# Performance work log

Hardware: AMD Instinct MI355X
Metric: run time of the kernel (lower is better)

## Reference

```python
import jax, jax.numpy as jnp
import numpy as np

NUM_USERS = 100000
NUM_ITEMS = 50000
EMBED = 64
S_NNZ = NUM_USERS * 32   # avg social degree 32
R_NNZ = NUM_USERS * 50   # avg 50 rated items per user
BATCH = 8192


def setup_inputs() -> dict:
    key = jax.random.key(0)
    ks = jax.random.split(key, 12)
    d = EMBED
    # Embedding tables (xavier-uniform style scale)
    U = jax.random.uniform(ks[0], (NUM_USERS, d), jnp.float32, -1.0, 1.0) * np.sqrt(6.0 / (NUM_USERS + d))
    V = jax.random.uniform(ks[1], (NUM_ITEMS, d), jnp.float32, -1.0, 1.0) * np.sqrt(6.0 / (NUM_ITEMS + d))
    # Diffusion layer weights: Linear(2d -> d). Stored as [2d, d] (x @ W + b).
    lim = np.sqrt(6.0 / (3 * d))
    W0 = jax.random.uniform(ks[2], (2 * d, d), jnp.float32, -lim, lim)
    b0 = jnp.zeros((d,), jnp.float32)
    W1 = jax.random.uniform(ks[3], (2 * d, d), jnp.float32, -lim, lim)
    b1 = jnp.zeros((d,), jnp.float32)
    # Sparse social matrix S [NUM_USERS, NUM_USERS], COO edge lists, row-normalized values.
    S_row = jax.random.randint(ks[4], (S_NNZ,), 0, NUM_USERS, jnp.int32)
    S_col = jax.random.randint(ks[5], (S_NNZ,), 0, NUM_USERS, jnp.int32)
    S_val = jnp.full((S_NNZ,), 1.0 / 32.0, jnp.float32)
    # Sparse rating matrix R [NUM_USERS, NUM_ITEMS]
    R_row = jax.random.randint(ks[6], (R_NNZ,), 0, NUM_USERS, jnp.int32)
    R_col = jax.random.randint(ks[7], (R_NNZ,), 0, NUM_ITEMS, jnp.int32)
    R_val = jnp.full((R_NNZ,), 1.0 / 50.0, jnp.float32)
    batch_user = jax.random.randint(ks[8], (BATCH,), 0, NUM_USERS, jnp.int64 if jax.config.jax_enable_x64 else jnp.int32)
    batch_pos_item = jax.random.randint(ks[9], (BATCH,), 0, NUM_ITEMS, jnp.int32)
    batch_neg_item = jax.random.randint(ks[10], (BATCH,), 0, NUM_ITEMS, jnp.int32)
    return dict(batch_user=batch_user, batch_pos_item=batch_pos_item, batch_neg_item=batch_neg_item,
                U=U, V=V, W0=W0, b0=b0, W1=W1, b1=b1,
                S_row=S_row, S_col=S_col, S_val=S_val,
                R_row=R_row, R_col=R_col, R_val=R_val)


def _spmm(row, col, val, X, n_rows):
    # (sparse [n_rows, n] COO) @ X : gather + scale + segment-sum
    return jax.ops.segment_sum(val[:, None] * X[col], row, num_segments=n_rows)


def reference(batch_user, batch_pos_item, batch_neg_item, U, V, W0, b0, W1, b1,
              S_row, S_col, S_val, R_row, R_col, R_val):
    # Diffusion layers: U <- relu(concat([S @ U, U]) @ W + b)
    for W, b in ((W0, b0), (W1, b1)):
        agg = _spmm(S_row, S_col, S_val, U, NUM_USERS)          # [num_users, d]
        U = jax.nn.relu(jnp.concatenate([agg, U], axis=1) @ W + b)
    user_g = U + _spmm(R_row, R_col, R_val, V, NUM_USERS)        # [num_users, d]
    bu = user_g[batch_user]          # [B, d]
    bp = V[batch_pos_item]           # [B, d]
    bn = V[batch_neg_item]           # [B, d]
    return (bu, bp, bn)
```

## Files before the change

### kernel.cpp

```cpp
#include <hip/hip_runtime.h>
#include <hip/hip_bf16.h>

#define NUM_USERS 100000
#define NUM_ITEMS 50000
#define EMBED     64
#define S_NNZ     (NUM_USERS * 32)
#define R_NNZ     (NUM_USERS * 50)
#define BATCH     8192

#define NB    256
#define NCH   256
#define CHUNK (S_NNZ / NCH)
#define BROWS 391


__global__ __launch_bounds__(256) void k_p1hist(const int* __restrict__ rows, int* __restrict__ cnt_t) {
    __shared__ int h[NB];
    int t = threadIdx.x, b = blockIdx.x;
    h[t] = 0;
    __syncthreads();
    int base = b * CHUNK;
    for (int i = t; i < CHUNK; i += 256) atomicAdd(&h[rows[base + i] / BROWS], 1);
    __syncthreads();
    cnt_t[t * NCH + b] = h[t];
}

__global__ __launch_bounds__(1024) void k_scan1(const int* __restrict__ cnt, int* __restrict__ excl,
                                                int* __restrict__ bsums, int n) {
    __shared__ int buf[1024];
    int t = threadIdx.x;
    int i = blockIdx.x * 1024 + t;
    int x = (i < n) ? cnt[i] : 0;
    buf[t] = x;
    __syncthreads();
    for (int off = 1; off < 1024; off <<= 1) {
        int y = (t >= off) ? buf[t - off] : 0;
        __syncthreads();
        buf[t] += y;
        __syncthreads();
    }
    if (i < n) excl[i] = buf[t] - x;
    if (t == 1023) bsums[blockIdx.x] = buf[1023];
}

__global__ __launch_bounds__(1024) void k_scan2(int* __restrict__ bsums, int nb, int* __restrict__ total_slot) {
    __shared__ int buf[1024];
    int t = threadIdx.x;
    int x = (t < nb) ? bsums[t] : 0;
    buf[t] = x;
    __syncthreads();
    for (int off = 1; off < 1024; off <<= 1) {
        int y = (t >= off) ? buf[t - off] : 0;
        __syncthreads();
        buf[t] += y;
        __syncthreads();
    }
    if (t < nb) bsums[t] = buf[t] - x;
    if (t == 1023) total_slot[0] = buf[1023];
}

__global__ void k_scan3b(int* __restrict__ a, const int* __restrict__ bsums, int n) {
    int i = blockIdx.x * blockDim.x + threadIdx.x;
    if (i < n) a[i] += bsums[i >> 10];
}

__global__ __launch_bounds__(256) void k_p1scatter(const int* __restrict__ rows, const int* __restrict__ cols,
                                                   const float* __restrict__ vals, const int* __restrict__ cnt_t,
                                                   int* __restrict__ tmpRow, int2* __restrict__ tmpCV) {
    __shared__ int cur[NB];
    int t = threadIdx.x, b = blockIdx.x;
    cur[t] = cnt_t[t * NCH + b];
    __syncthreads();
    int base = b * CHUNK;
    for (int i = t; i < CHUNK; i += 256) {
        int e = base + i;
        int r = rows[e];
        int pos = atomicAdd(&cur[r / BROWS], 1);
        tmpRow[pos] = r;
        tmpCV[pos]  = make_int2(cols[e], __float_as_int(vals[e]));
    }
}

__global__ __launch_bounds__(512) void k_p2(const int* __restrict__ tmpRow, const int2* __restrict__ tmpCV,
                                            const int* __restrict__ cnt_t,
                                            int* __restrict__ rowptr, int2* __restrict__ colval) {
    __shared__ int h[512];
    __shared__ int s[512];
    __shared__ int cur[BROWS + 1];
    int t = threadIdx.x, k = blockIdx.x;
    int beg = cnt_t[k * NCH];
    int end = (k < NB - 1) ? cnt_t[(k + 1) * NCH] : S_NNZ;
    h[t] = 0;
    __syncthreads();
    int rbase = k * BROWS;
    for (int j = beg + t; j < end; j += 512) atomicAdd(&h[tmpRow[j] - rbase], 1);
    __syncthreads();
    s[t] = h[t];
    __syncthreads();
    for (int off = 1; off < 512; off <<= 1) {
        int y = (t >= off) ? s[t - off] : 0;
        __syncthreads();
        s[t] += y;
        __syncthreads();
    }
    int excl = s[t] - h[t];
    int gr   = rbase + t;
    if (t <= BROWS && gr <= NUM_USERS) rowptr[gr] = beg + excl;
    if (t <= BROWS) cur[t] = beg + excl;
    __syncthreads();
    for (int j = beg + t; j < end; j += 512) {
        int pos = atomicAdd(&cur[tmpRow[j] - rbase], 1);
        colval[pos] = tmpCV[j];
    }
}

__global__ __launch_bounds__(256) void k_spmm_csr(const int* __restrict__ rowptr,
                                                  const int2* __restrict__ colval,
                                                  const float* __restrict__ X,
                                                  float* __restrict__ Y, int n_rows) {
    int w    = blockIdx.x * (blockDim.x >> 6) + (threadIdx.x >> 6);
    int lane = threadIdx.x & 63;
    if (w >= n_rows) return;
    int beg = rowptr[w], end = rowptr[w + 1];
    float acc = 0.0f;
    int j    = beg;
    int jend = beg + ((end - beg) & ~7);
    for (; j < jend; j += 8) {
        int2 cv[8];
#pragma unroll
        for (int u = 0; u < 8; ++u) cv[u] = colval[j + u];
        float x[8];
#pragma unroll
        for (int u = 0; u < 8; ++u) x[u] = X[(size_t)cv[u].x * EMBED + lane];
#pragma unroll
        for (int u = 0; u < 8; ++u) acc = fmaf(__int_as_float(cv[u].y), x[u], acc);
    }
    for (; j < end; ++j) acc = fmaf(__int_as_float(colval[j].y), X[(size_t)colval[j].x * EMBED + lane], acc);
    Y[(size_t)w * EMBED + lane] = acc;
}

__global__ __launch_bounds__(256) void k_spmm_batch(const int* __restrict__ rowptr,
                                                    const int2* __restrict__ colval,
                                                    const float* __restrict__ X,
                                                    const int* __restrict__ bu,
                                                    float* __restrict__ Agg2, int n) {
    int w    = blockIdx.x * (blockDim.x >> 6) + (threadIdx.x >> 6);
    int lane = threadIdx.x & 63;
    if (w >= n) return;
    int r   = bu[w];
    int beg = rowptr[r], end = rowptr[r + 1];
    float acc = 0.0f;
    int j    = beg;
    int jend = beg + ((end - beg) & ~7);
    for (; j < jend; j += 8) {
        int2 cv[8];
#pragma unroll
        for (int u = 0; u < 8; ++u) cv[u] = colval[j + u];
        float x[8];
#pragma unroll
        for (int u = 0; u < 8; ++u) x[u] = X[(size_t)cv[u].x * EMBED + lane];
#pragma unroll
        for (int u = 0; u < 8; ++u) acc = fmaf(__int_as_float(cv[u].y), x[u], acc);
    }
    for (; j < end; ++j) acc = fmaf(__int_as_float(colval[j].y), X[(size_t)colval[j].x * EMBED + lane], acc);
    Agg2[(size_t)w * EMBED + lane] = acc;
}

__global__ __launch_bounds__(256) void k_layer(const float* __restrict__ Agg,
                                               const float* __restrict__ Uin,
                                               float* __restrict__ Uout,
                                               const float* __restrict__ W,
                                               const float* __restrict__ b) {
    __shared__ float Wl[128 * 64];
    __shared__ float xs[16][128];
    int t = threadIdx.x;
    for (int i = t; i < 128 * 64; i += 256) Wl[i] = W[i];
    int rl = t >> 6;
    int c  = t & 63;
    int rbase = blockIdx.x * 16;
#pragma unroll
    for (int q = 0; q < 4; ++q) {
        int rr = rbase + rl * 4 + q;
        if (rr < NUM_USERS) {
            xs[rl * 4 + q][c]      = Agg[(size_t)rr * EMBED + c];
            xs[rl * 4 + q][64 + c] = Uin[(size_t)rr * EMBED + c];
        }
    }
    __syncthreads();
    float bias = b[c];
#pragma unroll
    for (int q = 0; q < 4; ++q) {
        int rr = rbase + rl * 4 + q;
        if (rr >= NUM_USERS) break;
        float acc = bias;
#pragma unroll
        for (int k = 0; k < 128; ++k) acc = fmaf(xs[rl * 4 + q][k], Wl[k * 64 + c], acc);
        Uout[(size_t)rr * EMBED + c] = fmaxf(acc, 0.0f);
    }
}

__global__ __launch_bounds__(256) void k_layer_batch(const float* __restrict__ Agg2,
                                                     const float* __restrict__ Uin,
                                                     const int* __restrict__ bu,
                                                     float* __restrict__ out0,
                                                     const float* __restrict__ W,
                                                     const float* __restrict__ b) {
    __shared__ float Wl[128 * 64];
    __shared__ float xs[16][128];
    int t = threadIdx.x;
    for (int i = t; i < 128 * 64; i += 256) Wl[i] = W[i];
    int rl = t >> 6;
    int c  = t & 63;
    int rbase = blockIdx.x * 16;
#pragma unroll
    for (int q = 0; q < 4; ++q) {
        int s = rbase + rl * 4 + q;
        if (s < BATCH) {
            xs[rl * 4 + q][c]      = Agg2[(size_t)s * EMBED + c];
            xs[rl * 4 + q][64 + c] = Uin[(size_t)bu[s] * EMBED + c];
        }
    }
    __syncthreads();
    float bias = b[c];
#pragma unroll
    for (int q = 0; q < 4; ++q) {
        int s = rbase + rl * 4 + q;
        if (s >= BATCH) break;
        float acc = bias;
#pragma unroll
        for (int k = 0; k < 128; ++k) acc = fmaf(xs[rl * 4 + q][k], Wl[k * 64 + c], acc);
        out0[(size_t)s * EMBED + c] = fmaxf(acc, 0.0f);
    }
}


__global__ void k_chain(const int* __restrict__ bu, int* __restrict__ head,
                        int* __restrict__ nxt, int n) {
    int i = blockIdx.x * blockDim.x + threadIdx.x;
    if (i < n) nxt[i] = atomicExch(&head[bu[i]], i);
}

__global__ __launch_bounds__(256) void k_filter(const int* __restrict__ rows,
                                                const int* __restrict__ cols,
                                                const float* __restrict__ vals,
                                                const int* __restrict__ head,
                                                const int* __restrict__ nxt,
                                                const float* __restrict__ V,
                                                float* __restrict__ out0, int nnz) {
    int e    = blockIdx.x * blockDim.x + threadIdx.x;
    int lane = threadIdx.x & 63;
    int r = (e < nnz) ? rows[e] : -1;
    int h = (r >= 0) ? head[r] : -1;
    unsigned long long mask = __ballot(h >= 0);
    int   c = 0;
    float v = 0.0f;
    if (h >= 0) { c = cols[e]; v = vals[e]; }
    while (mask) {
        int l = __ffsll((long long)mask) - 1;
        mask &= mask - 1;
        int   cc = __shfl(c, l);
        float vv = __shfl(v, l);
        int   hh = __shfl(h, l);
        float x  = vv * V[(size_t)cc * EMBED + lane];
        while (hh >= 0) {
            atomicAdd(&out0[(size_t)hh * EMBED + lane], x);
            hh = nxt[hh];
        }
    }
}

__global__ void k_gather2(const float* __restrict__ V,
                          const int* __restrict__ bp, const int* __restrict__ bn,
                          float* __restrict__ out) {
    int i = blockIdx.x * blockDim.x + threadIdx.x;
    if (i >= BATCH * EMBED) return;
    int row = i >> 6, l = i & 63;
    out[BATCH * EMBED + i]     = V[(size_t)bp[row] * EMBED + l];
    out[2 * BATCH * EMBED + i] = V[(size_t)bn[row] * EMBED + l];
}


extern "C" void kernel_launch(void* const* d_in, const int* in_sizes, int n_in,
                              void* d_out, int out_size, void* d_ws, size_t ws_size,
                              hipStream_t stream) {
    const int*   batch_user = (const int*)d_in[0];
    const int*   batch_pos  = (const int*)d_in[1];
    const int*   batch_neg  = (const int*)d_in[2];
    const float* U     = (const float*)d_in[3];
    const float* V     = (const float*)d_in[4];
    const float* W0    = (const float*)d_in[5];
    const float* b0    = (const float*)d_in[6];
    const float* W1    = (const float*)d_in[7];
    const float* b1    = (const float*)d_in[8];
    const int*   S_row = (const int*)d_in[9];
    const int*   S_col = (const int*)d_in[10];
    const float* S_val = (const float*)d_in[11];
    const int*   R_row = (const int*)d_in[12];
    const int*   R_col = (const int*)d_in[13];
    const float* R_val = (const float*)d_in[14];
    float* out = (float*)d_out;

    const size_t tabElems = (size_t)NUM_USERS * EMBED;

    char* wsb = (char*)d_ws;
    size_t o = 0;
    float* A       = (float*)(wsb + o); o += tabElems * 4;
    float* B       = (float*)(wsb + o); o += tabElems * 4;
    float* Agg2    = (float*)(wsb + o); o += (size_t)BATCH * EMBED * 4;
    int*   rowptrS = (int*)(wsb + o);   o += (NUM_USERS + 1) * 4;
    int*   cnt_t   = (int*)(wsb + o);   o += (size_t)NB * NCH * 4;
    int*   bsums   = (int*)(wsb + o);   o += 1024 * 4;
    int*   head    = (int*)(wsb + o);   o += NUM_USERS * 4;
    int*   nxt     = (int*)(wsb + o);   o += BATCH * 4;
    o = (o + 7) & ~(size_t)7;
    int2*  colvalS = (int2*)(wsb + o);  o += (size_t)S_NNZ * 8;

    int*  tmpRow = (int*)A;
    int2* tmpCV  = (int2*)B;

    const int spmm_blocks  = (NUM_USERS * 64 + 255) / 256;
    const int layer_blocks = (NUM_USERS + 15) / 16;

    k_p1hist<<<NCH, 256, 0, stream>>>(S_row, cnt_t);
    k_scan1<<<(NB * NCH) / 1024, 1024, 0, stream>>>(cnt_t, cnt_t, bsums, NB * NCH);
    k_scan2<<<1, 1024, 0, stream>>>(bsums, (NB * NCH) / 1024, &bsums[512]);
    k_scan3b<<<(NB * NCH) / 256, 256, 0, stream>>>(cnt_t, bsums, NB * NCH);
    k_p1scatter<<<NCH, 256, 0, stream>>>(S_row, S_col, S_val, cnt_t, tmpRow, tmpCV);
    k_p2<<<NB, 512, 0, stream>>>(tmpRow, tmpCV, cnt_t, rowptrS, colvalS);

    k_spmm_csr<<<spmm_blocks, 256, 0, stream>>>(rowptrS, colvalS, U, B, NUM_USERS);
    k_layer<<<layer_blocks, 256, 0, stream>>>(B, U, A, W0, b0);

    hipMemsetAsync(head, 0xFF, NUM_USERS * sizeof(int), stream);
    k_chain<<<(BATCH + 255) / 256, 256, 0, stream>>>(batch_user, head, nxt, BATCH);

    k_spmm_batch<<<(BATCH * 64 + 255) / 256, 256, 0, stream>>>(rowptrS, colvalS, A, batch_user, Agg2, BATCH);
    k_layer_batch<<<(BATCH + 15) / 16, 256, 0, stream>>>(Agg2, A, batch_user, out, W1, b1);

    k_filter<<<(R_NNZ + 255) / 256, 256, 0, stream>>>(R_row, R_col, R_val, head, nxt, V, out, R_NNZ);

    k_gather2<<<(BATCH * EMBED + 255) / 256, 256, 0, stream>>>(V, batch_pos, batch_neg, out);
}
```

Measured before the change: 622.2 us.

## Gather bf16 embedding copies in SpMM/filter and pack row offsets into edge temp

Converts U, the layer-0 output and V into bf16 shadow tables, and the SpMM and rating-filter kernels now gather from those, halving the bytes per random row gather. The CSR build packs the local row offset into the high bits of the column word, so the temporary edge buffer is one int2 array instead of separate row and column/value arrays. This adds conversion kernels and an extra bf16 store in the layer kernel, and gathered values lose precision, which may exceed tolerance.

New measurement: 599.3 us. -3.7%, faster.

```diff
diff --git a/kernel.cpp b/kernel.cpp
--- a/kernel.cpp
+++ b/kernel.cpp
@@ -66,34 +66,32 @@
 
 __global__ __launch_bounds__(256) void k_p1scatter(const int* __restrict__ rows, const int* __restrict__ cols,
                                                    const float* __restrict__ vals, const int* __restrict__ cnt_t,
-                                                   int* __restrict__ tmpRow, int2* __restrict__ tmpCV) {
+                                                   int2* __restrict__ tmpE) {
     __shared__ int cur[NB];
     int t = threadIdx.x, b = blockIdx.x;
     cur[t] = cnt_t[t * NCH + b];
     __syncthreads();
     int base = b * CHUNK;
     for (int i = t; i < CHUNK; i += 256) {
-        int e = base + i;
-        int r = rows[e];
-        int pos = atomicAdd(&cur[r / BROWS], 1);
-        tmpRow[pos] = r;
-        tmpCV[pos]  = make_int2(cols[e], __float_as_int(vals[e]));
-    }
-}
-
-__global__ __launch_bounds__(512) void k_p2(const int* __restrict__ tmpRow, const int2* __restrict__ tmpCV,
-                                            const int* __restrict__ cnt_t,
+        int e  = base + i;
+        int r  = rows[e];
+        int bk = r / BROWS;
+        int pos = atomicAdd(&cur[bk], 1);
+        tmpE[pos] = make_int2(((r - bk * BROWS) << 17) | cols[e], __float_as_int(vals[e]));
+    }
+}
+
+__global__ __launch_bounds__(512) void k_p2(const int2* __restrict__ tmpE, const int* __restrict__ cnt_t,
                                             int* __restrict__ rowptr, int2* __restrict__ colval) {
     __shared__ int h[512];
     __shared__ int s[512];
-    __shared__ int cur[BROWS + 1];
+    __shared__ int cur[512];
     int t = threadIdx.x, k = blockIdx.x;
     int beg = cnt_t[k * NCH];
     int end = (k < NB - 1) ? cnt_t[(k + 1) * NCH] : S_NNZ;
     h[t] = 0;
     __syncthreads();
-    int rbase = k * BROWS;
-    for (int j = beg + t; j < end; j += 512) atomicAdd(&h[tmpRow[j] - rbase], 1);
+    for (int j = beg + t; j < end; j += 512) atomicAdd(&h[((unsigned)tmpE[j].x) >> 17], 1);
     __syncthreads();
     s[t] = h[t];
     __syncthreads();
@@ -104,20 +102,26 @@
         __syncthreads();
     }
     int excl = s[t] - h[t];
-    int gr   = rbase + t;
+    int gr   = k * BROWS + t;
     if (t <= BROWS && gr <= NUM_USERS) rowptr[gr] = beg + excl;
-    if (t <= BROWS) cur[t] = beg + excl;
+    cur[t] = beg + excl;
     __syncthreads();
     for (int j = beg + t; j < end; j += 512) {
-        int pos = atomicAdd(&cur[tmpRow[j] - rbase], 1);
-        colval[pos] = tmpCV[j];
-    }
-}
-
-__global__ __launch_bounds__(256) void k_spmm_csr(const int* __restrict__ rowptr,
-                                                  const int2* __restrict__ colval,
-                                                  const float* __restrict__ X,
-                                                  float* __restrict__ Y, int n_rows) {
+        int2 e  = tmpE[j];
+        int pos = atomicAdd(&cur[((unsigned)e.x) >> 17], 1);
+        colval[pos] = make_int2(e.x & 0x1FFFF, e.y);
+    }
+}
+
+__global__ void k_cvt(const float* __restrict__ src, __hip_bfloat16* __restrict__ dst, int n) {
+    int i = blockIdx.x * blockDim.x + threadIdx.x;
+    if (i < n) dst[i] = __float2bfloat16(src[i]);
+}
+
+__global__ __launch_bounds__(256) void k_spmm16(const int* __restrict__ rowptr,
+                                                const int2* __restrict__ colval,
+                                                const __hip_bfloat16* __restrict__ X,
+                                                float* __restrict__ Y, int n_rows) {
     int w    = blockIdx.x * (blockDim.x >> 6) + (threadIdx.x >> 6);
     int lane = threadIdx.x & 63;
     if (w >= n_rows) return;
@@ -131,19 +135,20 @@
         for (int u = 0; u < 8; ++u) cv[u] = colval[j + u];
         float x[8];
 #pragma unroll
-        for (int u = 0; u < 8; ++u) x[u] = X[(size_t)cv[u].x * EMBED + lane];
+        for (int u = 0; u < 8; ++u) x[u] = __bfloat162float(X[(size_t)cv[u].x * EMBED + lane]);
 #pragma unroll
         for (int u = 0; u < 8; ++u) acc = fmaf(__int_as_float(cv[u].y), x[u], acc);
     }
-    for (; j < end; ++j) acc = fmaf(__int_as_float(colval[j].y), X[(size_t)colval[j].x * EMBED + lane], acc);
+    for (; j < end; ++j)
+        acc = fmaf(__int_as_float(colval[j].y), __bfloat162float(X[(size_t)colval[j].x * EMBED + lane]), acc);
     Y[(size_t)w * EMBED + lane] = acc;
 }
 
-__global__ __launch_bounds__(256) void k_spmm_batch(const int* __restrict__ rowptr,
-                                                    const int2* __restrict__ colval,
-                                                    const float* __restrict__ X,
-                                                    const int* __restrict__ bu,
-                                                    float* __restrict__ Agg2, int n) {
+__global__ __launch_bounds__(256) void k_spmm_batch16(const int* __restrict__ rowptr,
+                                                      const int2* __restrict__ colval,
+                                                      const __hip_bfloat16* __restrict__ X,
+                                                      const int* __restrict__ bu,
+                                                      float* __restrict__ Agg2, int n) {
     int w    = blockIdx.x * (blockDim.x >> 6) + (threadIdx.x >> 6);
     int lane = threadIdx.x & 63;
     if (w >= n) return;
@@ -158,17 +163,19 @@
         for (int u = 0; u < 8; ++u) cv[u] = colval[j + u];
         float x[8];
 #pragma unroll
-        for (int u = 0; u < 8; ++u) x[u] = X[(size_t)cv[u].x * EMBED + lane];
+        for (int u = 0; u < 8; ++u) x[u] = __bfloat162float(X[(size_t)cv[u].x * EMBED + lane]);
 #pragma unroll
         for (int u = 0; u < 8; ++u) acc = fmaf(__int_as_float(cv[u].y), x[u], acc);
     }
-    for (; j < end; ++j) acc = fmaf(__int_as_float(colval[j].y), X[(size_t)colval[j].x * EMBED + lane], acc);
+    for (; j < end; ++j)
+        acc = fmaf(__int_as_float(colval[j].y), __bfloat162float(X[(size_t)colval[j].x * EMBED + lane]), acc);
     Agg2[(size_t)w * EMBED + lane] = acc;
 }
 
 __global__ __launch_bounds__(256) void k_layer(const float* __restrict__ Agg,
                                                const float* __restrict__ Uin,
                                                float* __restrict__ Uout,
+                                               __hip_bfloat16* __restrict__ Uout16,
                                                const float* __restrict__ W,
                                                const float* __restrict__ b) {
     __shared__ float Wl[128 * 64];
@@ -195,7 +202,9 @@
         float acc = bias;
 #pragma unroll
         for (int k = 0; k < 128; ++k) acc = fmaf(xs[rl * 4 + q][k], Wl[k * 64 + c], acc);
-        Uout[(size_t)rr * EMBED + c] = fmaxf(acc, 0.0f);
+        float v = fmaxf(acc, 0.0f);
+        Uout[(size_t)rr * EMBED + c]   = v;
+        Uout16[(size_t)rr * EMBED + c] = __float2bfloat16(v);
     }
 }
 
@@ -240,13 +249,13 @@
     if (i < n) nxt[i] = atomicExch(&head[bu[i]], i);
 }
 
-__global__ __launch_bounds__(256) void k_filter(const int* __restrict__ rows,
-                                                const int* __restrict__ cols,
-                                                const float* __restrict__ vals,
-                                                const int* __restrict__ head,
-                                                const int* __restrict__ nxt,
-                                                const float* __restrict__ V,
-                                                float* __restrict__ out0, int nnz) {
+__global__ __launch_bounds__(256) void k_filter16(const int* __restrict__ rows,
+                                                  const int* __restrict__ cols,
+                                                  const float* __restrict__ vals,
+                                                  const int* __restrict__ head,
+                                                  const int* __restrict__ nxt,
+                                                  const __hip_bfloat16* __restrict__ V16,
+                                                  float* __restrict__ out0, int nnz) {
     int e    = blockIdx.x * blockDim.x + threadIdx.x;
     int lane = threadIdx.x & 63;
     int r = (e < nnz) ? rows[e] : -1;
@@ -261,7 +270,7 @@
         int   cc = __shfl(c, l);
         float vv = __shfl(v, l);
         int   hh = __shfl(h, l);
-        float x  = vv * V[(size_t)cc * EMBED + lane];
+        float x  = vv * __bfloat162float(V16[(size_t)cc * EMBED + lane]);
         while (hh >= 0) {
             atomicAdd(&out0[(size_t)hh * EMBED + lane], x);
             hh = nxt[hh];
@@ -314,9 +323,9 @@
     int*   nxt     = (int*)(wsb + o);   o += BATCH * 4;
     o = (o + 7) & ~(size_t)7;
     int2*  colvalS = (int2*)(wsb + o);  o += (size_t)S_NNZ * 8;
-
-    int*  tmpRow = (int*)A;
-    int2* tmpCV  = (int2*)B;
+    __hip_bfloat16* X16 = (__hip_bfloat16*)(wsb + o); o += tabElems * 2;
+
+    int2* tmpE = (int2*)A;
 
     const int spmm_blocks  = (NUM_USERS * 64 + 255) / 256;
     const int layer_blocks = (NUM_USERS + 15) / 16;
@@ -325,19 +334,21 @@
     k_scan1<<<(NB * NCH) / 1024, 1024, 0, stream>>>(cnt_t, cnt_t, bsums, NB * NCH);
     k_scan2<<<1, 1024, 0, stream>>>(bsums, (NB * NCH) / 1024, &bsums[512]);
     k_scan3b<<<(NB * NCH) / 256, 256, 0, stream>>>(cnt_t, bsums, NB * NCH);
-    k_p1scatter<<<NCH, 256, 0, stream>>>(S_row, S_col, S_val, cnt_t, tmpRow, tmpCV);
-    k_p2<<<NB, 512, 0, stream>>>(tmpRow, tmpCV, cnt_t, rowptrS, colvalS);
-
-    k_spmm_csr<<<spmm_blocks, 256, 0, stream>>>(rowptrS, colvalS, U, B, NUM_USERS);
-    k_layer<<<layer_blocks, 256, 0, stream>>>(B, U, A, W0, b0);
+    k_p1scatter<<<NCH, 256, 0, stream>>>(S_row, S_col, S_val, cnt_t, tmpE);
+    k_p2<<<NB, 512, 0, stream>>>(tmpE, cnt_t, rowptrS, colvalS);
+
+    k_cvt<<<(int)((tabElems + 255) / 256), 256, 0, stream>>>(U, X16, (int)tabElems);
+    k_spmm16<<<spmm_blocks, 256, 0, stream>>>(rowptrS, colvalS, X16, B, NUM_USERS);
+    k_layer<<<layer_blocks, 256, 0, stream>>>(B, U, A, X16, W0, b0);
 
     hipMemsetAsync(head, 0xFF, NUM_USERS * sizeof(int), stream);
     k_chain<<<(BATCH + 255) / 256, 256, 0, stream>>>(batch_user, head, nxt, BATCH);
 
-    k_spmm_batch<<<(BATCH * 64 + 255) / 256, 256, 0, stream>>>(rowptrS, colvalS, A, batch_user, Agg2, BATCH);
+    k_spmm_batch16<<<(BATCH * 64 + 255) / 256, 256, 0, stream>>>(rowptrS, colvalS, X16, batch_user, Agg2, BATCH);
     k_layer_batch<<<(BATCH + 15) / 16, 256, 0, stream>>>(Agg2, A, batch_user, out, W1, b1);
 
-    k_filter<<<(R_NNZ + 255) / 256, 256, 0, stream>>>(R_row, R_col, R_val, head, nxt, V, out, R_NNZ);
+    k_cvt<<<(int)(((size_t)NUM_ITEMS * EMBED + 255) / 256), 256, 0, stream>>>(V, X16, NUM_ITEMS * EMBED);
+    k_filter16<<<(R_NNZ + 255) / 256, 256, 0, stream>>>(R_row, R_col, R_val, head, nxt, X16, out, R_NNZ);
 
     k_gather2<<<(BATCH * EMBED + 255) / 256, 256, 0, stream>>>(V, batch_pos, batch_neg, out);
 }
```
